# Performance work log

Hardware: AMD Instinct MI355X
Metric: run time of the kernel (lower is better)

The kernel has to match this reference:

```python
import jax, jax.numpy as jnp
import numpy as np
import math

B, S, H, HN, D = 4, 1024, 1024, 16, 64  # batch, seq, hidden, heads, head_dim

def setup_inputs() -> dict:
    key = jax.random.key(0)
    ks = jax.random.split(key, 12)
    w = lambda k, shp: (jax.random.normal(k, shp, dtype=jnp.float32) * 0.02)
    return {
        "key": jax.random.normal(ks[0], (B, S, H), dtype=jnp.float32),
        "value": jax.random.normal(ks[1], (B, S, H), dtype=jnp.float32),
        "query": jax.random.normal(ks[2], (B, S, H), dtype=jnp.float32),
        "mask": jnp.zeros((B, 1, S, S), dtype=jnp.float32),
        "position_bias": jax.random.normal(ks[3], (1, HN, S, S), dtype=jnp.float32),
        "prev_attn": jax.random.normal(ks[4], (B, HN, S, S), dtype=jnp.float32),
        "Wq": w(ks[5], (H, HN * D)), "bq": jnp.zeros((HN * D,), jnp.float32),
        "Wk": w(ks[6], (H, HN * D)), "bk": jnp.zeros((HN * D,), jnp.float32),
        "Wv": w(ks[7], (H, HN * D)), "bv": jnp.zeros((HN * D,), jnp.float32),
        "Wo": w(ks[8], (HN * D, H)), "bo": jnp.zeros((H,), jnp.float32),
    }

def reference(key, value, query, mask, position_bias, prev_attn,
              Wq, bq, Wk, bk, Wv, bv, Wo, bo):
    b, s, _ = query.shape
    # QKV projections -> [b, heads, s, d]
    q = (query @ Wq + bq).reshape(b, s, HN, D).transpose(0, 2, 1, 3)
    k = (key @ Wk + bk).reshape(b, s, HN, D).transpose(0, 2, 1, 3)
    v = (value @ Wv + bv).reshape(b, s, HN, D).transpose(0, 2, 1, 3)
    scores = jnp.einsum('bhqd,bhkd->bhqk', q, k)
    # note: position_bias is added BEFORE the 1/sqrt(d) scaling, as in the source
    scores = (scores + position_bias) / math.sqrt(float(D))
    scores = scores + mask
    scores = scores + prev_attn  # has_residual_attention=True path
    prev_attn_out = scores
    probs = jax.nn.softmax(scores, axis=-1)  # dropout p=0.0 -> identity
    ctx = jnp.einsum('bhqk,bhkd->bqhd', probs, v).reshape(b, s, HN * D)
    output = ctx @ Wo + bo
    return (output, prev_attn_out)
```

## Files before the change

kernel.cpp:

```cpp
#include <hip/hip_runtime.h>
#include <hip/hip_bf16.h>
#include <cstdint>

typedef unsigned short u16;
typedef unsigned int u32;

#define BB   4
#define SSQ  1024
#define HHD  1024
#define HNN  16
#define DDIM 64
#define MM   (BB*SSQ)
#define OUT0_ELEMS ((size_t)MM*HHD)
#define SLP  68
#define GST  56

typedef __attribute__((ext_vector_type(8))) short  short8;
typedef __attribute__((ext_vector_type(8))) __bf16 bf16x8;
typedef __attribute__((ext_vector_type(4))) float  f32x4;
typedef __attribute__((ext_vector_type(4))) u16    u16x4;

__device__ __forceinline__ u16 f2b(float f) {
    u32 u = __builtin_bit_cast(u32, f);
    u += 0x7FFFu + ((u >> 16) & 1u);
    return (u16)(u >> 16);
}
__device__ __forceinline__ bf16x8 ld8(const u16* p) {
    return *(const bf16x8*)p;
}
__device__ __forceinline__ f32x4 ldnt4(const float* p) {
    return __builtin_nontemporal_load((const f32x4*)p);
}
__device__ __forceinline__ f32x4 mfma16(bf16x8 a, bf16x8 b, f32x4 c) {
    return __builtin_amdgcn_mfma_f32_16x16x32_bf16(a, b, c, 0, 0, 0);
}

__global__ void conv_x(const float* __restrict__ q, const float* __restrict__ k,
                       const float* __restrict__ v, u16* __restrict__ out) {
    int z = blockIdx.z;
    const float* src = (z == 0) ? q : (z == 1) ? k : v;
    size_t i = (size_t)blockIdx.x * blockDim.x + threadIdx.x;
    f32x4 f = ((const f32x4*)src)[i];
    u16x4 o;
    o[0] = f2b(f[0]); o[1] = f2b(f[1]); o[2] = f2b(f[2]); o[3] = f2b(f[3]);
    ((u16x4*)(out + (size_t)z * MM * HHD))[i] = o;
}

__global__ void conv_wt(const float* __restrict__ w0, const float* __restrict__ w1,
                        const float* __restrict__ w2, const float* __restrict__ w3,
                        u16* __restrict__ out) {
    __shared__ float t[32][33];
    int z = blockIdx.z;
    const float* src = (z == 0) ? w0 : (z == 1) ? w1 : (z == 2) ? w2 : w3;
    int k0 = blockIdx.y * 32, n0 = blockIdx.x * 32;
    int tx = threadIdx.x, ty = threadIdx.y;
    for (int i = ty; i < 32; i += 8)
        t[i][tx] = src[(size_t)(k0 + i) * HHD + n0 + tx];
    __syncthreads();
    u16* dst = out + (size_t)z * HHD * HHD;
    for (int i = ty; i < 32; i += 8)
        dst[(size_t)(n0 + i) * HHD + k0 + tx] = f2b(t[tx][i]);
}

__global__ __launch_bounds__(256) void gemm_xw(
        const u16* __restrict__ Xb, const u16* __restrict__ Wt,
        const float* __restrict__ bq, const float* __restrict__ bk,
        const float* __restrict__ bv,
        u16* __restrict__ qh, u16* __restrict__ kh, u16* __restrict__ vt) {
    __shared__ u16 As[128 * GST];
    __shared__ u16 Bs[128 * GST];
    int z = blockIdx.z;
    const u16* X = Xb + (size_t)z * MM * HHD;
    const u16* W = Wt + (size_t)z * HHD * HHD;
    const float* bias = (z == 0) ? bq : (z == 1) ? bk : bv;
    int tid = threadIdx.x;
    int lane = tid & 63, w = tid >> 6;
    int wm = w >> 1, wn = w & 1;
    int rbase = blockIdx.y * 128, cbase = blockIdx.x * 128;
    int lr = lane & 15, lg = lane >> 4;
    int row0 = tid >> 2, q0 = tid & 3;
    int row1 = (tid + 256) >> 2, q1 = tid & 3;
    f32x4 acc[4][4] = {};
    for (int k0 = 0; k0 < HHD; k0 += 32) {
        f32x4 ra0 = *(const f32x4*)(X + (size_t)(rbase + row0) * HHD + k0 + q0 * 8);
        f32x4 rb0 = *(const f32x4*)(W + (size_t)(cbase + row0) * HHD + k0 + q0 * 8);
        f32x4 ra1 = *(const f32x4*)(X + (size_t)(rbase + row1) * HHD + k0 + q1 * 8);
        f32x4 rb1 = *(const f32x4*)(W + (size_t)(cbase + row1) * HHD + k0 + q1 * 8);
        __syncthreads();
        *(f32x4*)(&As[row0 * GST + q0 * 8]) = ra0;
        *(f32x4*)(&Bs[row0 * GST + q0 * 8]) = rb0;
        *(f32x4*)(&As[row1 * GST + q1 * 8]) = ra1;
        *(f32x4*)(&Bs[row1 * GST + q1 * 8]) = rb1;
        __syncthreads();
        bf16x8 a[4], b[4];
#pragma unroll
        for (int i = 0; i < 4; i++)
            a[i] = *(const bf16x8*)(&As[(wm * 64 + i * 16 + lr) * GST + lg * 8]);
#pragma unroll
        for (int j = 0; j < 4; j++)
            b[j] = *(const bf16x8*)(&Bs[(wn * 64 + j * 16 + lr) * GST + lg * 8]);
#pragma unroll
        for (int i = 0; i < 4; i++)
#pragma unroll
            for (int j = 0; j < 4; j++)
                acc[i][j] = mfma16(a[i], b[j], acc[i][j]);
    }
    int rw = rbase + wm * 64, cw = cbase + wn * 64;
#pragma unroll
    for (int i = 0; i < 4; i++)
#pragma unroll
        for (int j = 0; j < 4; j++) {
            int col = cw + j * 16 + lr;
            float bval = bias[col];
            int h = col >> 6, d = col & 63;
#pragma unroll
            for (int e = 0; e < 4; e++) {
                int row = rw + i * 16 + lg * 4 + e;
                int bidx = row >> 10, s = row & 1023;
                u16 o = f2b(acc[i][j][e] + bval);
                if (z == 0)
                    qh[(((size_t)bidx * HNN + h) * SSQ + s) * DDIM + d] = o;
                else if (z == 1)
                    kh[(((size_t)bidx * HNN + h) * SSQ + s) * DDIM + d] = o;
                else
                    vt[(((size_t)bidx * HNN + h) * DDIM + d) * SSQ + s] = o;
            }
        }
}

__global__ __launch_bounds__(256) void attn_fused(
        const u16* __restrict__ qh, const u16* __restrict__ kh,
        const u16* __restrict__ vt,
        const float* __restrict__ pb, const float* __restrict__ mask,
        const float* __restrict__ prev,
        float* __restrict__ out_sc, u16* __restrict__ ctx) {
    __shared__ float slw[4 * 16 * SLP];
    __shared__ u16   pfw[4 * 16 * 64];
    __shared__ float lsw[64];
    int bh = blockIdx.y;
    int b = bh >> 4, h = bh & 15;
    int rbase0 = blockIdx.x * 64;
    int tid = threadIdx.x, lane = tid & 63, w = tid >> 6;
    int lr = lane & 15, lg = lane >> 4;
    int wr = w * 16;

    const u16* Q = qh + (size_t)bh * SSQ * DDIM;
    const u16* K = kh + (size_t)bh * SSQ * DDIM;
    const u16* V = vt + (size_t)bh * DDIM * SSQ;
    const float* pbh = pb + (size_t)h * SSQ * SSQ;
    const float* mb  = mask + (size_t)b * SSQ * SSQ;
    const float* pr  = prev + (size_t)bh * SSQ * SSQ;
    float* ob = out_sc + (size_t)bh * SSQ * SSQ;

    float* ws = slw + w * 16 * SLP;
    char* pslice = (char*)pfw + w * 2048;

    bf16x8 aq[2];
#pragma unroll
    for (int ks = 0; ks < 2; ks++)
        aq[ks] = ld8(Q + (size_t)(rbase0 + wr + lr) * DDIM + ks * 32 + lg * 8);

    f32x4 acc_pv[4] = {};
    float seacc[4] = {0.f, 0.f, 0.f, 0.f};

    for (int kt = 0; kt < 16; ++kt) {
        int cb = kt * 64;
        size_t eidx = (size_t)(rbase0 + wr + lg) * SSQ + cb + lr * 4;
        f32x4 pF = *(const f32x4*)(pbh + eidx);
        f32x4 mF = *(const f32x4*)(mb + eidx);
        f32x4 rF = ldnt4(pr + eidx);
        bf16x8 bv[4][2];
#pragma unroll
        for (int j = 0; j < 4; j++)
#pragma unroll
            for (int ks = 0; ks < 2; ks++)
                bv[j][ks] = ld8(V + (size_t)(j * 16 + lr) * SSQ + cb + ks * 32 + lg * 8);
        bf16x8 bk[4][2];
#pragma unroll
        for (int j = 0; j < 4; j++)
#pragma unroll
            for (int ks = 0; ks < 2; ks++)
                bk[j][ks] = ld8(K + (size_t)(cb + j * 16 + lr) * DDIM + ks * 32 + lg * 8);
        f32x4 acc_s[4] = {};
#pragma unroll
        for (int ks = 0; ks < 2; ks++)
#pragma unroll
            for (int j = 0; j < 4; j++)
                acc_s[j] = mfma16(aq[ks], bk[j][ks], acc_s[j]);
#pragma unroll
        for (int j = 0; j < 4; j++)
#pragma unroll
            for (int e = 0; e < 4; e++)
                ws[(lg * 4 + e) * SLP + j * 16 + lr] = acc_s[j][e];

#pragma unroll
        for (int it = 0; it < 4; ++it) {
            int rl = it * 4 + lg;
            size_t idx = (size_t)(rbase0 + wr + rl) * SSQ + cb + lr * 4;
            f32x4 p4 = pF, m4 = mF, r4 = rF;
            if (it < 3) {
                size_t idx2 = idx + (size_t)4 * SSQ;
                pF = *(const f32x4*)(pbh + idx2);
                mF = *(const f32x4*)(mb + idx2);
                rF = ldnt4(pr + idx2);
            }
            f32x4 s4 = *(const f32x4*)(ws + rl * SLP + lr * 4);
            f32x4 o4;
#pragma unroll
            for (int c = 0; c < 4; c++)
                o4[c] = (s4[c] + p4[c]) * 0.125f + m4[c] + r4[c];
            __builtin_nontemporal_store(o4, (f32x4*)(ob + idx));
            f32x4 e4;
#pragma unroll
            for (int c = 0; c < 4; c++) e4[c] = __expf(o4[c]);
            u16x4 pk;
#pragma unroll
            for (int c = 0; c < 4; c++) pk[c] = f2b(e4[c]);
            int byte = (rl * 128 + lr * 8) ^ ((rl & 7) << 4);
            *(u16x4*)(pslice + byte) = pk;
            float se = e4[0] + e4[1] + e4[2] + e4[3];
#pragma unroll
            for (int off = 8; off >= 1; off >>= 1) se += __shfl_xor(se, off);
            seacc[it] += se;
        }

        bf16x8 a[2];
#pragma unroll
        for (int ks = 0; ks < 2; ks++) {
            int byte = (lr * 128 + ks * 64 + lg * 16) ^ ((lr & 7) << 4);
            a[ks] = *(const bf16x8*)(pslice + byte);
        }
#pragma unroll
        for (int j = 0; j < 4; j++)
#pragma unroll
            for (int ks = 0; ks < 2; ks++)
                acc_pv[j] = mfma16(a[ks], bv[j][ks], acc_pv[j]);
    }

    if (lr == 0) {
#pragma unroll
        for (int it = 0; it < 4; ++it)
            lsw[wr + it * 4 + lg] = seacc[it];
    }
    float linv[4];
#pragma unroll
    for (int e = 0; e < 4; e++)
        linv[e] = 1.f / lsw[wr + lg * 4 + e];
#pragma unroll
    for (int j = 0; j < 4; j++) {
        int d = j * 16 + lr;
#pragma unroll
        for (int e = 0; e < 4; e++) {
            int row = rbase0 + wr + lg * 4 + e;
            ctx[((size_t)(b * SSQ + row)) * HHD + h * DDIM + d] =
                f2b(acc_pv[j][e] * linv[e]);
        }
    }
}

__global__ __launch_bounds__(256) void gemm_out(
        const u16* __restrict__ ctxb, const u16* __restrict__ WtO,
        const float* __restrict__ bo, float* __restrict__ out) {
    __shared__ u16 As[128 * GST];
    __shared__ u16 Bs[128 * GST];
    int tid = threadIdx.x;
    int lane = tid & 63, w = tid >> 6;
    int wm = w >> 1, wn = w & 1;
    int rbase = blockIdx.y * 128, cbase = blockIdx.x * 128;
    int lr = lane & 15, lg = lane >> 4;
    int row0 = tid >> 2, q0 = tid & 3;
    int row1 = (tid + 256) >> 2, q1 = tid & 3;
    f32x4 acc[4][4] = {};
    for (int k0 = 0; k0 < HHD; k0 += 32) {
        f32x4 ra0 = *(const f32x4*)(ctxb + (size_t)(rbase + row0) * HHD + k0 + q0 * 8);
        f32x4 rb0 = *(const f32x4*)(WtO + (size_t)(cbase + row0) * HHD + k0 + q0 * 8);
        f32x4 ra1 = *(const f32x4*)(ctxb + (size_t)(rbase + row1) * HHD + k0 + q1 * 8);
        f32x4 rb1 = *(const f32x4*)(WtO + (size_t)(cbase + row1) * HHD + k0 + q1 * 8);
        __syncthreads();
        *(f32x4*)(&As[row0 * GST + q0 * 8]) = ra0;
        *(f32x4*)(&Bs[row0 * GST + q0 * 8]) = rb0;
        *(f32x4*)(&As[row1 * GST + q1 * 8]) = ra1;
        *(f32x4*)(&Bs[row1 * GST + q1 * 8]) = rb1;
        __syncthreads();
        bf16x8 a[4], b[4];
#pragma unroll
        for (int i = 0; i < 4; i++)
            a[i] = *(const bf16x8*)(&As[(wm * 64 + i * 16 + lr) * GST + lg * 8]);
#pragma unroll
        for (int j = 0; j < 4; j++)
            b[j] = *(const bf16x8*)(&Bs[(wn * 64 + j * 16 + lr) * GST + lg * 8]);
#pragma unroll
        for (int i = 0; i < 4; i++)
#pragma unroll
            for (int j = 0; j < 4; j++)
                acc[i][j] = mfma16(a[i], b[j], acc[i][j]);
    }
    int rw = rbase + wm * 64, cw = cbase + wn * 64;
#pragma unroll
    for (int i = 0; i < 4; i++)
#pragma unroll
        for (int j = 0; j < 4; j++) {
            int col = cw + j * 16 + lr;
            float bval = bo[col];
#pragma unroll
            for (int e = 0; e < 4; e++) {
                int row = rw + i * 16 + lg * 4 + e;
                out[(size_t)row * HHD + col] = acc[i][j][e] + bval;
            }
        }
}

extern "C" void kernel_launch(void* const* d_in, const int* in_sizes, int n_in,
                              void* d_out, int out_size, void* d_ws, size_t ws_size,
                              hipStream_t stream) {
    const float* key   = (const float*)d_in[0];
    const float* value = (const float*)d_in[1];
    const float* query = (const float*)d_in[2];
    const float* mask  = (const float*)d_in[3];
    const float* pb    = (const float*)d_in[4];
    const float* prev  = (const float*)d_in[5];
    const float* Wq    = (const float*)d_in[6];
    const float* bq    = (const float*)d_in[7];
    const float* Wk    = (const float*)d_in[8];
    const float* bk    = (const float*)d_in[9];
    const float* Wv    = (const float*)d_in[10];
    const float* bv    = (const float*)d_in[11];
    const float* Wo    = (const float*)d_in[12];
    const float* bo    = (const float*)d_in[13];

    u16* Xb  = (u16*)d_ws;
    u16* Wt  = Xb + (size_t)3 * MM * HHD;
    u16* qh  = Wt + (size_t)4 * HHD * HHD;
    u16* kh  = qh + (size_t)MM * HHD;
    u16* vt  = kh + (size_t)MM * HHD;
    u16* ctx = vt + (size_t)MM * HHD;

    float* out0 = (float*)d_out;
    float* sc   = out0 + OUT0_ELEMS;

    conv_x<<<dim3(4096, 1, 3), 256, 0, stream>>>(query, key, value, Xb);
    conv_wt<<<dim3(32, 32, 4), dim3(32, 8), 0, stream>>>(Wq, Wk, Wv, Wo, Wt);
    gemm_xw<<<dim3(8, 32, 3), 256, 0, stream>>>(Xb, Wt, bq, bk, bv, qh, kh, vt);
    attn_fused<<<dim3(16, 64), 256, 0, stream>>>(qh, kh, vt, pb, mask, prev, sc, ctx);
    gemm_out<<<dim3(8, 32), 256, 0, stream>>>(ctx, Wt + (size_t)3 * HHD * HHD, bo, out0);
}
```

Before: 330.4 us.

## Split attention key range across two blocks and combine partial contexts

The fused attention kernel now runs with a third grid dimension that splits the 1024 keys into two halves. Each block writes an unnormalized bf16 partial context and per-row partial exp-sums, and a new pv_combine kernel adds the two partials and divides by the total sum. The aim is more independent blocks, for better latency hiding and less tail imbalance on the memory-bound score pass. In exchange it adds an extra launch and an extra round trip of partial-context traffic, and rounding the unnormalized partials to bf16 costs some precision.

```diff
diff --git a/kernel.cpp b/kernel.cpp
--- a/kernel.cpp
+++ b/kernel.cpp
@@ -24,6 +24,10 @@
     u32 u = __builtin_bit_cast(u32, f);
     u += 0x7FFFu + ((u >> 16) & 1u);
     return (u16)(u >> 16);
+}
+__device__ __forceinline__ float b2f(u16 v) {
+    u32 u = ((u32)v) << 16;
+    return __builtin_bit_cast(float, u);
 }
 __device__ __forceinline__ bf16x8 ld8(const u16* p) {
     return *(const bf16x8*)p;
@@ -133,13 +137,15 @@
         const u16* __restrict__ vt,
         const float* __restrict__ pb, const float* __restrict__ mask,
         const float* __restrict__ prev,
-        float* __restrict__ out_sc, u16* __restrict__ ctx) {
+        float* __restrict__ out_sc, u16* __restrict__ pctxb,
+        float* __restrict__ lp) {
     __shared__ float slw[4 * 16 * SLP];
     __shared__ u16   pfw[4 * 16 * 64];
-    __shared__ float lsw[64];
     int bh = blockIdx.y;
     int b = bh >> 4, h = bh & 15;
     int rbase0 = blockIdx.x * 64;
+    int z = blockIdx.z;
+    int kb0 = z * 512;
     int tid = threadIdx.x, lane = tid & 63, w = tid >> 6;
     int lr = lane & 15, lg = lane >> 4;
     int wr = w * 16;
@@ -151,6 +157,7 @@
     const float* mb  = mask + (size_t)b * SSQ * SSQ;
     const float* pr  = prev + (size_t)bh * SSQ * SSQ;
     float* ob = out_sc + (size_t)bh * SSQ * SSQ;
+    u16* pctx = pctxb + (size_t)z * MM * HHD;
 
     float* ws = slw + w * 16 * SLP;
     char* pslice = (char*)pfw + w * 2048;
@@ -163,8 +170,8 @@
     f32x4 acc_pv[4] = {};
     float seacc[4] = {0.f, 0.f, 0.f, 0.f};
 
-    for (int kt = 0; kt < 16; ++kt) {
-        int cb = kt * 64;
+    for (int kt = 0; kt < 8; ++kt) {
+        int cb = kb0 + kt * 64;
         size_t eidx = (size_t)(rbase0 + wr + lg) * SSQ + cb + lr * 4;
         f32x4 pF = *(const f32x4*)(pbh + eidx);
         f32x4 mF = *(const f32x4*)(mb + eidx);
@@ -240,22 +247,37 @@
     if (lr == 0) {
 #pragma unroll
         for (int it = 0; it < 4; ++it)
-            lsw[wr + it * 4 + lg] = seacc[it];
-    }
-    float linv[4];
-#pragma unroll
-    for (int e = 0; e < 4; e++)
-        linv[e] = 1.f / lsw[wr + lg * 4 + e];
+            lp[((size_t)z * 64 + bh) * SSQ + rbase0 + wr + it * 4 + lg] = seacc[it];
+    }
 #pragma unroll
     for (int j = 0; j < 4; j++) {
         int d = j * 16 + lr;
 #pragma unroll
         for (int e = 0; e < 4; e++) {
             int row = rbase0 + wr + lg * 4 + e;
-            ctx[((size_t)(b * SSQ + row)) * HHD + h * DDIM + d] =
-                f2b(acc_pv[j][e] * linv[e]);
-        }
-    }
+            pctx[((size_t)(b * SSQ + row)) * HHD + h * DDIM + d] = f2b(acc_pv[j][e]);
+        }
+    }
+}
+
+__global__ __launch_bounds__(256) void pv_combine(
+        const u16* __restrict__ pctxb, const float* __restrict__ lp,
+        u16* __restrict__ ctx) {
+    size_t i4 = (size_t)blockIdx.x * 256 + threadIdx.x;
+    size_t i = i4 * 4;
+    int b   = (int)(i >> 22);
+    int row = (int)(i >> 10) & 1023;
+    int h   = (int)(i >> 6) & 15;
+    int bh = b * 16 + h;
+    float l = lp[(size_t)bh * SSQ + row] + lp[((size_t)64 + bh) * SSQ + row];
+    float linv = 1.f / l;
+    u16x4 c0 = ((const u16x4*)pctxb)[i4];
+    u16x4 c1 = ((const u16x4*)(pctxb + (size_t)MM * HHD))[i4];
+    u16x4 o;
+#pragma unroll
+    for (int c = 0; c < 4; c++)
+        o[c] = f2b((b2f(c0[c]) + b2f(c1[c])) * linv);
+    ((u16x4*)ctx)[i4] = o;
 }
 
 __global__ __launch_bounds__(256) void gemm_out(
@@ -334,6 +356,8 @@
     u16* kh  = qh + (size_t)MM * HHD;
     u16* vt  = kh + (size_t)MM * HHD;
     u16* ctx = vt + (size_t)MM * HHD;
+    u16*   pctx = (u16*)d_ws;
+    float* lp   = (float*)(pctx + (size_t)2 * MM * HHD);
 
     float* out0 = (float*)d_out;
     float* sc   = out0 + OUT0_ELEMS;
@@ -341,6 +365,7 @@
     conv_x<<<dim3(4096, 1, 3), 256, 0, stream>>>(query, key, value, Xb);
     conv_wt<<<dim3(32, 32, 4), dim3(32, 8), 0, stream>>>(Wq, Wk, Wv, Wo, Wt);
     gemm_xw<<<dim3(8, 32, 3), 256, 0, stream>>>(Xb, Wt, bq, bk, bv, qh, kh, vt);
-    attn_fused<<<dim3(16, 64), 256, 0, stream>>>(qh, kh, vt, pb, mask, prev, sc, ctx);
+    attn_fused<<<dim3(16, 64, 2), 256, 0, stream>>>(qh, kh, vt, pb, mask, prev, sc, pctx, lp);
+    pv_combine<<<dim3(4096), 256, 0, stream>>>(pctx, lp, ctx);
     gemm_out<<<dim3(8, 32), 256, 0, stream>>>(ctx, Wt + (size_t)3 * HHD * HHD, bo, out0);
 }
```

Result: slower. 345.3 us (+4.5%).
